# Kernel tuning notes

Hardware: AMD Instinct MI355X
Metric: run time of the kernel (lower is better)

The kernel has to match this reference:

```python
import jax, jax.numpy as jnp
import numpy as np

N_NODES = 1_000_000   # nodal points, 3 DOFs each
N_ELEMS = 500_000     # H8 (8-node hexahedral) elements
N_TYPES = 64          # distinct element stiffness matrices (24x24)


def setup_inputs() -> dict:
    key = jax.random.key(0)
    k1, k2, k3, k4 = jax.random.split(key, 4)
    U = jax.random.normal(k1, (N_NODES, 3), dtype=jnp.float32)
    filters = jax.random.normal(k2, (N_TYPES, 24, 24), dtype=jnp.float32)
    H8types = jax.random.randint(k3, (N_ELEMS,), 0, N_TYPES, dtype=jnp.int32)
    nodIdx = jax.random.randint(k4, (N_ELEMS, 8), 0, N_NODES, dtype=jnp.int32)
    return {"U": U, "filters": filters, "H8types": H8types, "nodIdx": nodIdx}


def reference(U, filters, H8types, nodIdx):
    """FEM stiffness matvec KU = sum_e scatter(K_type(e) @ gather(U, e)).

    U:       [N, 3]      nodal displacements (3 DOFs per node)
    filters: [T, 24, 24] per-type element stiffness matrices
    H8types: [E]         element type index into filters
    nodIdx:  [E, 8]      element -> node connectivity
    returns KU: [N, 3]
    """
    E = nodIdx.shape[0]
    # gather the 8 nodes x 3 DOFs of each element -> [E, 24]
    ue = U[nodIdx].reshape(E, 24)
    # per-type stiffness for each element -> [E, 24, 24]
    Ke = filters[H8types]
    # per-element force vector f_e = K_e @ u_e -> [E, 24]
    fe = jnp.einsum('eij,ej->ei', Ke, ue)
    # scatter-add element forces back to nodal DOFs
    KU = jnp.zeros_like(U).at[nodIdx.reshape(-1)].add(fe.reshape(E * 8, 3))
    return KU
```

## Files before the change

kernel.cpp:

```cpp
#include <hip/hip_runtime.h>


#define NTYPES    64
#define KSTRIDE   580
#define RSHIFT    11
#define RNODES    2048
#define MAXB      512
#define CAP       10240
#define K1_TPB    1024
#define K1_EPT    2
#define K1_CHUNK  (K1_TPB * K1_EPT)
#define K2_TPB    1024
#define PREP_TPB  256

typedef int          nint4  __attribute__((ext_vector_type(4)));
typedef unsigned int nuint2 __attribute__((ext_vector_type(2)));
typedef unsigned int nuint4 __attribute__((ext_vector_type(4)));

__device__ __forceinline__ unsigned bf16_rne(float f) {
    unsigned b = __float_as_uint(f);
    return (b + 0x7FFFu + ((b >> 16) & 1u)) >> 16;
}


__global__ __launch_bounds__(PREP_TPB) void pack_u_kernel(
    const float* __restrict__ U, nuint2* __restrict__ Ub,
    float* __restrict__ KU, unsigned* __restrict__ tails,
    int n_nodes, int n_buckets)
{
    int n = blockIdx.x * PREP_TPB + threadIdx.x;
    if (n < n_buckets) tails[n] = 0;
    if (n >= n_nodes) return;
    const float* up = U + (size_t)n * 3;
    unsigned bx = bf16_rne(up[0]);
    unsigned by = bf16_rne(up[1]);
    unsigned bz = bf16_rne(up[2]);
    nuint2 v = { bx | (by << 16), bz };
    Ub[n] = v;
    KU[3 * n + 0] = 0.f;
    KU[3 * n + 1] = 0.f;
    KU[3 * n + 2] = 0.f;
}


__global__ __launch_bounds__(K1_TPB, 4) void feconv_bin_kernel(
    const nuint2* __restrict__ Ub,
    const float* __restrict__ K,
    const int*   __restrict__ types,
    const int*   __restrict__ nodIdx,
    float*       __restrict__ KU,
    unsigned*    __restrict__ tails,
    nuint2*      __restrict__ recs,
    int n_elems, int n_buckets)
{
    extern __shared__ float sK[];
    __shared__ unsigned sCnt[MAXB];
    __shared__ unsigned sBase[MAXB];

    for (int w = threadIdx.x; w < NTYPES * 576; w += K1_TPB) {
        int t = w / 576;
        int r = w - t * 576;
        sK[t * KSTRIDE + r] = K[w];
    }
    for (int i = threadIdx.x; i < n_buckets; i += K1_TPB) sCnt[i] = 0;
    __syncthreads();

    const int e0 = blockIdx.x * K1_CHUNK + threadIdx.x;
    int     nodes[K1_EPT][8];
    int     tt[K1_EPT];
    nuint2  uu[K1_EPT][8];

#pragma unroll
    for (int k = 0; k < K1_EPT; ++k) {
        int e = e0 + k * K1_TPB;
        tt[k] = -1;
        if (e < n_elems) {
            tt[k] = __builtin_nontemporal_load(&types[e]);
            const nint4* q = (const nint4*)(nodIdx + (size_t)e * 8);
            nint4 a = __builtin_nontemporal_load(q);
            nint4 b = __builtin_nontemporal_load(q + 1);
            nodes[k][0] = a.x; nodes[k][1] = a.y; nodes[k][2] = a.z; nodes[k][3] = a.w;
            nodes[k][4] = b.x; nodes[k][5] = b.y; nodes[k][6] = b.z; nodes[k][7] = b.w;
#pragma unroll
            for (int j = 0; j < 8; ++j)
                uu[k][j] = Ub[nodes[k][j]];
#pragma unroll
            for (int j = 0; j < 8; ++j)
                atomicAdd(&sCnt[(unsigned)nodes[k][j] >> RSHIFT], 1u);
        }
    }
    __syncthreads();

    for (int b = threadIdx.x; b < n_buckets; b += K1_TPB) {
        unsigned c = sCnt[b];
        sBase[b] = c ? atomicAdd(&tails[b], c) : 0u;
        sCnt[b] = 0;
    }
    __syncthreads();

#pragma unroll
    for (int k = 0; k < K1_EPT; ++k) {
        if (tt[k] < 0) continue;

        float ue[24];
#pragma unroll
        for (int j = 0; j < 8; ++j) {
            nuint2 v = uu[k][j];
            ue[3 * j + 0] = __uint_as_float(v.x << 16);
            ue[3 * j + 1] = __uint_as_float(v.x & 0xFFFF0000u);
            ue[3 * j + 2] = __uint_as_float(v.y << 16);
        }

        const float4* Kt4 = (const float4*)(sK + tt[k] * KSTRIDE);
#pragma unroll
        for (int j = 0; j < 8; ++j) {
            float a0 = 0.f, a1 = 0.f, a2 = 0.f;
#pragma unroll
            for (int q = 0; q < 6; ++q) {
                float4 k0 = Kt4[(3 * j + 0) * 6 + q];
                float4 k1 = Kt4[(3 * j + 1) * 6 + q];
                float4 k2 = Kt4[(3 * j + 2) * 6 + q];
                float u0 = ue[4 * q + 0], u1 = ue[4 * q + 1];
                float u2 = ue[4 * q + 2], u3 = ue[4 * q + 3];
                a0 += k0.x * u0 + k0.y * u1 + k0.z * u2 + k0.w * u3;
                a1 += k1.x * u0 + k1.y * u1 + k1.z * u2 + k1.w * u3;
                a2 += k2.x * u0 + k2.y * u1 + k2.z * u2 + k2.w * u3;
            }
            unsigned n = (unsigned)nodes[k][j];
            unsigned b = n >> RSHIFT;
            unsigned pos = sBase[b] + atomicAdd(&sCnt[b], 1u);
            if (pos < CAP) {
                unsigned local = n & (RNODES - 1);
                nuint2 r = { bf16_rne(a0) | (bf16_rne(a1) << 16),
                             bf16_rne(a2) | (local << 16) };
                recs[(size_t)b * CAP + pos] = r;
            } else {
                atomicAdd(&KU[(size_t)n * 3 + 0], a0);
                atomicAdd(&KU[(size_t)n * 3 + 1], a1);
                atomicAdd(&KU[(size_t)n * 3 + 2], a2);
            }
        }
    }
}


__global__ __launch_bounds__(K2_TPB) void feconv_acc_kernel(
    const nuint2*   __restrict__ recs,
    const unsigned* __restrict__ tails,
    float*          __restrict__ KU,
    int n_nodes)
{
    __shared__ float sAcc[RNODES * 3];
    const int b = blockIdx.x;

    for (int i = threadIdx.x; i < RNODES * 3; i += K2_TPB) sAcc[i] = 0.f;
    __syncthreads();

    unsigned cnt = tails[b];
    if (cnt > CAP) cnt = CAP;
    const nuint2* base = recs + (size_t)b * CAP;
    const nuint4* base4 = (const nuint4*)base;

    unsigned npairs = cnt >> 1;
    for (unsigned i = threadIdx.x; i < npairs; i += K2_TPB) {
        nuint4 p = base4[i];
        unsigned o0 = (p.y >> 16) * 3;
        atomicAdd(&sAcc[o0 + 0], __uint_as_float(p.x << 16));
        atomicAdd(&sAcc[o0 + 1], __uint_as_float(p.x & 0xFFFF0000u));
        atomicAdd(&sAcc[o0 + 2], __uint_as_float(p.y << 16));
        unsigned o1 = (p.w >> 16) * 3;
        atomicAdd(&sAcc[o1 + 0], __uint_as_float(p.z << 16));
        atomicAdd(&sAcc[o1 + 1], __uint_as_float(p.z & 0xFFFF0000u));
        atomicAdd(&sAcc[o1 + 2], __uint_as_float(p.w << 16));
    }
    if ((cnt & 1u) && threadIdx.x == 0) {
        nuint2 r = base[cnt - 1];
        unsigned o = (r.y >> 16) * 3;
        atomicAdd(&sAcc[o + 0], __uint_as_float(r.x << 16));
        atomicAdd(&sAcc[o + 1], __uint_as_float(r.x & 0xFFFF0000u));
        atomicAdd(&sAcc[o + 2], __uint_as_float(r.y << 16));
    }
    __syncthreads();

    const int nbase = b * RNODES;
    int limit = n_nodes - nbase;
    if (limit > RNODES) limit = RNODES;
    limit *= 3;
    float* out = KU + (size_t)nbase * 3;
    for (int i = threadIdx.x; i < limit; i += K2_TPB) out[i] += sAcc[i];
}


__global__ __launch_bounds__(256) void feconv_elem_kernel(
    const float* __restrict__ U, const float* __restrict__ K,
    const int* __restrict__ types, const int* __restrict__ nodIdx,
    float* __restrict__ KU, int n_elems)
{
    int e = blockIdx.x * blockDim.x + threadIdx.x;
    if (e >= n_elems) return;
    int t = types[e];
    const int4* idx4 = (const int4*)(nodIdx + (size_t)e * 8);
    int4 iA = idx4[0], iB = idx4[1];
    int nodes[8] = {iA.x, iA.y, iA.z, iA.w, iB.x, iB.y, iB.z, iB.w};
    float ue[24];
#pragma unroll
    for (int j = 0; j < 8; ++j) {
        const float* up = U + (size_t)nodes[j] * 3;
        ue[3 * j + 0] = up[0]; ue[3 * j + 1] = up[1]; ue[3 * j + 2] = up[2];
    }
    const float* Kt = K + (size_t)t * 576;
#pragma unroll
    for (int i = 0; i < 24; ++i) {
        const float4* row = (const float4*)(Kt + i * 24);
        float acc = 0.f;
#pragma unroll
        for (int q = 0; q < 6; ++q) {
            float4 k = row[q];
            acc += k.x * ue[4 * q + 0] + k.y * ue[4 * q + 1]
                 + k.z * ue[4 * q + 2] + k.w * ue[4 * q + 3];
        }
        atomicAdd(&KU[(size_t)nodes[i / 3] * 3 + (i % 3)], acc);
    }
}

extern "C" void kernel_launch(void* const* d_in, const int* in_sizes, int n_in,
                              void* d_out, int out_size, void* d_ws, size_t ws_size,
                              hipStream_t stream) {
    const float* U      = (const float*)d_in[0];
    const float* Kf     = (const float*)d_in[1];
    const int*   types  = (const int*)d_in[2];
    const int*   nodIdx = (const int*)d_in[3];
    float*       KU     = (float*)d_out;

    const int n_elems = in_sizes[2];
    const int n_nodes = in_sizes[0] / 3;
    const int n_buckets = (n_nodes + RNODES - 1) / RNODES;

    const size_t ub_off  = 4096;
    const size_t rec_off = ub_off + (((size_t)n_nodes * 8 + 255) & ~255ull);
    const size_t need    = rec_off + (size_t)n_buckets * CAP * 8;

    if (n_buckets <= MAXB && ws_size >= need) {
        unsigned* tails = (unsigned*)d_ws;
        nuint2*   Ub    = (nuint2*)((char*)d_ws + ub_off);
        nuint2*   recs  = (nuint2*)((char*)d_ws + rec_off);

        int gridP = (n_nodes + PREP_TPB - 1) / PREP_TPB;
        pack_u_kernel<<<gridP, PREP_TPB, 0, stream>>>(
            U, Ub, KU, tails, n_nodes, n_buckets);

        size_t lds_bytes = (size_t)NTYPES * KSTRIDE * sizeof(float);
        int grid1 = (n_elems + K1_CHUNK - 1) / K1_CHUNK;
        feconv_bin_kernel<<<grid1, K1_TPB, lds_bytes, stream>>>(
            Ub, Kf, types, nodIdx, KU, tails, recs, n_elems, n_buckets);
        feconv_acc_kernel<<<n_buckets, K2_TPB, 0, stream>>>(
            recs, tails, KU, n_nodes);
    } else {
        (void)hipMemsetAsync(KU, 0, (size_t)out_size * sizeof(float), stream);
        int block = 256;
        int grid = (n_elems + block - 1) / block;
        feconv_elem_kernel<<<grid, block, 0, stream>>>(
            U, Kf, types, nodIdx, KU, n_elems);
    }
}
```

Baseline: 212.0 us.

## Sort elements by type within each block chunk before matvec

Each block first counts element types in its chunk, prefix-sums the counts, and builds a permutation that groups elements of the same type together. Threads then process elements in this order, so a wavefront's stiffness-matrix reads from shared memory mostly hit the same type and serve as broadcasts. This adds several barriers, shared atomics and extra LDS. The nodIdx loads become scattered within the chunk and lose the nontemporal hint.

Measured after the change: 214.2 us. No clear change (+1.0%).

```diff
diff --git a/kernel.cpp b/kernel.cpp
--- a/kernel.cpp
+++ b/kernel.cpp
@@ -54,8 +54,12 @@
     int n_elems, int n_buckets)
 {
     extern __shared__ float sK[];
-    __shared__ unsigned sCnt[MAXB];
-    __shared__ unsigned sBase[MAXB];
+    __shared__ unsigned       sCnt[MAXB];
+    __shared__ unsigned       sBase[MAXB];
+    __shared__ unsigned       sTCnt[NTYPES];
+    __shared__ unsigned       sTOff[NTYPES];
+    __shared__ unsigned short sOrder[K1_CHUNK];
+    __shared__ unsigned char  sType[K1_CHUNK];
 
     for (int w = threadIdx.x; w < NTYPES * 576; w += K1_TPB) {
         int t = w / 576;
@@ -63,22 +67,65 @@
         sK[t * KSTRIDE + r] = K[w];
     }
     for (int i = threadIdx.x; i < n_buckets; i += K1_TPB) sCnt[i] = 0;
-    __syncthreads();
-
-    const int e0 = blockIdx.x * K1_CHUNK + threadIdx.x;
+    if (threadIdx.x < NTYPES) sTCnt[threadIdx.x] = 0;
+    __syncthreads();
+
+    const int base = blockIdx.x * K1_CHUNK;
+    int cnt_chunk = n_elems - base;
+    if (cnt_chunk > K1_CHUNK) cnt_chunk = K1_CHUNK;
+
+    int myT[K1_EPT];
+#pragma unroll
+    for (int k = 0; k < K1_EPT; ++k) {
+        int li = threadIdx.x + k * K1_TPB;
+        myT[k] = -1;
+        if (li < cnt_chunk) {
+            int t = __builtin_nontemporal_load(&types[base + li]);
+            myT[k] = t;
+            sType[li] = (unsigned char)t;
+            atomicAdd(&sTCnt[t], 1u);
+        }
+    }
+    __syncthreads();
+
+    if (threadIdx.x < NTYPES) {
+        unsigned v = sTCnt[threadIdx.x];
+        unsigned s = v;
+#pragma unroll
+        for (int d = 1; d < NTYPES; d <<= 1) {
+            unsigned o = __shfl_up(s, d, 64);
+            if ((int)threadIdx.x >= d) s += o;
+        }
+        sTOff[threadIdx.x] = s - v;
+        sTCnt[threadIdx.x] = 0;
+    }
+    __syncthreads();
+
+#pragma unroll
+    for (int k = 0; k < K1_EPT; ++k) {
+        int li = threadIdx.x + k * K1_TPB;
+        if (myT[k] >= 0) {
+            unsigned p = sTOff[myT[k]] + atomicAdd(&sTCnt[myT[k]], 1u);
+            sOrder[p] = (unsigned short)li;
+        }
+    }
+    __syncthreads();
+
     int     nodes[K1_EPT][8];
     int     tt[K1_EPT];
     nuint2  uu[K1_EPT][8];
 
 #pragma unroll
     for (int k = 0; k < K1_EPT; ++k) {
-        int e = e0 + k * K1_TPB;
+        int slot = threadIdx.x + k * K1_TPB;
         tt[k] = -1;
-        if (e < n_elems) {
-            tt[k] = __builtin_nontemporal_load(&types[e]);
+        if (slot < cnt_chunk) {
+            int li = sOrder[slot];
+            int e  = base + li;
+            tt[k] = sType[li];
             const nint4* q = (const nint4*)(nodIdx + (size_t)e * 8);
-            nint4 a = __builtin_nontemporal_load(q);
-            nint4 b = __builtin_nontemporal_load(q + 1);
+            nint4 a = q[0];
+            nint4 b = q[1];
             nodes[k][0] = a.x; nodes[k][1] = a.y; nodes[k][2] = a.z; nodes[k][3] = a.w;
             nodes[k][4] = b.x; nodes[k][5] = b.y; nodes[k][6] = b.z; nodes[k][7] = b.w;
 #pragma unroll
```
